# Kernel tuning notes

Hardware: AMD Instinct MI355X
Metric: run time of the kernel (lower is better)

## Reference

```python
import jax, jax.numpy as jnp
import numpy as np

ALPHA = 0.25
GAMMA = 2.0
IMG = 512.0


def _focal(t, logits):
    # faithful to get_focal_loss: sigmoid -> alpha/focal weighting -> BCE -> mean
    c = jax.nn.sigmoid(logits)
    alpha_factor = jnp.where(t == 1.0, ALPHA, 1.0 - ALPHA)
    focal_weight = alpha_factor * jnp.where(t == 1.0, 1.0 - c, c) ** GAMMA
    bce = -(t * jnp.log(c) + (1.0 - t) * jnp.log(1.0 - c))
    return (focal_weight * bce).mean()


def setup_inputs() -> dict:
    key = jax.random.key(0)
    kc, kr, kd, ka1, ka2, kb1, kb2, kl = jax.random.split(key, 8)
    B, A, C = 32, 200000, 10000
    classifications = jax.random.normal(kc, (B, C), dtype=jnp.float32)
    regressions = 0.1 * jax.random.normal(kr, (B, A, 4), dtype=jnp.float32)
    box_dist = jax.random.normal(kd, (B, A), dtype=jnp.float32)
    # anchors: random boxes inside a 512x512 image
    ctr = jax.random.uniform(ka1, (A, 2), minval=0.0, maxval=IMG)
    wh = jax.random.uniform(ka2, (A, 2), minval=16.0, maxval=256.0)
    anchor = jnp.concatenate([ctr - 0.5 * wh, ctr + 0.5 * wh], axis=1)
    anchors = anchor[None].astype(jnp.float32)  # [1, A, 4]
    # annotations: [B, 1, 7] = one gt box + 3 noun class indices (stored as float)
    gctr = jax.random.uniform(kb1, (B, 1, 2), minval=128.0, maxval=384.0)
    gwh = jax.random.uniform(kb2, (B, 1, 2), minval=64.0, maxval=256.0)
    gbox = jnp.concatenate([gctr - 0.5 * gwh, gctr + 0.5 * gwh], axis=2)
    nouns = jax.random.randint(kl, (B, 1, 3), 0, C).astype(jnp.float32)
    annotations = jnp.concatenate([gbox, nouns], axis=2).astype(jnp.float32)
    return {
        "classifications": classifications,
        "regressions": regressions,
        "box_dist": box_dist,
        "anchors": anchors,
        "annotations": annotations,
    }


def reference(classifications, regressions, box_dist, anchors, annotations):
    anchor = anchors[0]                              # [A, 4]
    aw = anchor[:, 2] - anchor[:, 0]
    ah = anchor[:, 3] - anchor[:, 1]
    ax = anchor[:, 0] + 0.5 * aw
    ay = anchor[:, 1] + 0.5 * ah
    area_a = aw * ah
    scale = jnp.array([0.1, 0.1, 0.2, 0.2], dtype=jnp.float32)

    def per_image(cls_j, reg_j, bd_j, ann_j):
        ann = ann_j[0]                               # [7] single annotation
        nouns = ann[4:7].astype(jnp.int32)
        target_nouns = jnp.zeros_like(cls_j).at[nouns].set(1.0)
        cls_loss = _focal(target_nouns, cls_j)
        # IoU of all anchors vs the single gt box; argmax over 1 box == box 0
        b = ann[:4]
        iw = jnp.clip(jnp.minimum(anchor[:, 2], b[2]) - jnp.maximum(anchor[:, 0], b[0]), 0.0)
        ih = jnp.clip(jnp.minimum(anchor[:, 3], b[3]) - jnp.maximum(anchor[:, 1], b[1]), 0.0)
        inter = iw * ih
        ua = jnp.clip(area_a + (b[2] - b[0]) * (b[3] - b[1]) - inter, 1e-8)
        iou_max = inter / ua                          # [A]
        pos = (iou_max >= 0.5).astype(cls_j.dtype)    # [A] float 0/1
        bbox_loss = _focal(pos, bd_j)
        # Faithful to the torch code: positive_indices.long() used as GATHER indices
        pidx = pos.astype(jnp.int32)                  # values in {0,1}
        aw_pi = aw[pidx]; ah_pi = ah[pidx]
        ax_pi = ax[pidx]; ay_pi = ay[pidx]
        # assigned_annotations rows are all identical (single gt, argmax==0),
        # so the 0/1 gather is an identity on the gt box
        gw_raw = b[2] - b[0]
        gh_raw = b[3] - b[1]
        gx = b[0] + 0.5 * gw_raw
        gy = b[1] + 0.5 * gh_raw
        gw = jnp.clip(gw_raw, 1.0)
        gh = jnp.clip(gh_raw, 1.0)
        targets = jnp.stack(
            [(gx - ax_pi) / aw_pi,
             (gy - ay_pi) / ah_pi,
             jnp.log(gw / aw_pi),
             jnp.log(gh / ah_pi)], axis=1) / scale    # [A, 4]
        diff = jnp.abs(targets - reg_j[pidx])
        rl = jnp.where(diff <= 1.0 / 9.0, 0.5 * 9.0 * diff ** 2, diff - 0.5 / 9.0).mean()
        reg_loss = jnp.where(pidx.sum() > 0, rl, jnp.zeros((), rl.dtype))
        return cls_loss, bbox_loss, reg_loss

    cl, bl, rl = jax.vmap(per_image)(classifications, regressions, box_dist, annotations)
    return (cl.mean(keepdims=True), bl.mean(keepdims=True), rl.mean(keepdims=True))
```

## Files before the change

kernel.cpp:

```cpp
#include <hip/hip_runtime.h>

#define B_IMG 32
#define N_A   200000
#define N_C   10000

#define NCH    60
#define BCH    3328
#define NCC    4
#define CCH    2560
#define SLOTS  64
#define GRID   (B_IMG * SLOTS)

#define WS_FOCAL 0
#define WS_CNT   (B_IMG * NCH)
#define WS_CLS   (2 * B_IMG * NCH)

typedef float f4 __attribute__((ext_vector_type(4)));

__device__ __forceinline__ float focal_elem(float x, bool t) {
    float e = __expf(-x);
    float r = __builtin_amdgcn_rcpf(1.0f + e);
    float L = __logf(1.0f + e);
    if (t) { float om = e * r; return 0.25f * om * om * L; }
    else   { return 0.75f * r * r * (x + L); }
}

__device__ __forceinline__ double wave_red(double v) {
#pragma unroll
    for (int o = 32; o; o >>= 1) v += __shfl_down(v, o, 64);
    return v;
}

__global__ __launch_bounds__(256) void main_kernel(
    const float* __restrict__ cls, const float* __restrict__ bd,
    const float* __restrict__ anc, const float* __restrict__ ann,
    double* __restrict__ ws)
{
    const int tid = threadIdx.x;
    const int lane = tid & 63, wv = tid >> 6;
    const int j  = blockIdx.x >> 6;
    const int ch = blockIdx.x & 63;
    __shared__ double sred[2][4];
    const f4* __restrict__ anc4 = (const f4*)anc;

    if (ch < NCH) {
        const int a0 = ch * BCH;
        const int a1 = (ch == NCH - 1) ? N_A : (a0 + BCH);
        const int nfull = (a1 - a0) >> 8;
        const float b0 = ann[j*7+0], b1 = ann[j*7+1], b2 = ann[j*7+2], b3 = ann[j*7+3];
        const float barea = (b2 - b0) * (b3 - b1);
        const float* __restrict__ bdr = bd + (size_t)j * N_A;

        float fsum = 0.0f, cnt = 0.0f;
        const int base = a0 + tid;
#pragma unroll 4
        for (int u = 0; u < nfull; ++u) {
            const int i = base + (u << 8);
            const f4 av = anc4[i];
            float iw = fmaxf(fminf(av.z, b2) - fmaxf(av.x, b0), 0.0f);
            float ih = fmaxf(fminf(av.w, b3) - fmaxf(av.y, b1), 0.0f);
            float inter = iw * ih;
            float ua = fmaxf((av.z - av.x) * (av.w - av.y) + barea - inter, 1e-8f);
            bool pos = (2.0f * inter >= ua);
            fsum += focal_elem(bdr[i], pos);
            cnt  += pos ? 1.0f : 0.0f;
        }
        {
            const int i = base + (nfull << 8);
            if (i < a1) {
                const f4 av = anc4[i];
                float iw = fmaxf(fminf(av.z, b2) - fmaxf(av.x, b0), 0.0f);
                float ih = fmaxf(fminf(av.w, b3) - fmaxf(av.y, b1), 0.0f);
                float inter = iw * ih;
                float ua = fmaxf((av.z - av.x) * (av.w - av.y) + barea - inter, 1e-8f);
                bool pos = (2.0f * inter >= ua);
                fsum += focal_elem(bdr[i], pos);
                cnt  += pos ? 1.0f : 0.0f;
            }
        }
        double fv = wave_red((double)fsum);
        double cv = wave_red((double)cnt);
        if (lane == 0) { sred[0][wv] = fv; sred[1][wv] = cv; }
        __syncthreads();
        if (tid == 0) {
            ws[WS_FOCAL + j * NCH + ch] = sred[0][0] + sred[0][1] + sred[0][2] + sred[0][3];
            ws[WS_CNT   + j * NCH + ch] = sred[1][0] + sred[1][1] + sred[1][2] + sred[1][3];
        }
    } else {
        const int cc = ch - NCH;
        const int c0 = cc * CCH;
        const int c1 = (cc == NCC - 1) ? N_C : (c0 + CCH);
        const int nfull = (c1 - c0) >> 8;
        const int n0 = (int)ann[j*7+4], n1 = (int)ann[j*7+5], n2 = (int)ann[j*7+6];
        const float* __restrict__ cj = cls + (size_t)j * N_C;
        float fsum = 0.0f;
        const int base = c0 + tid;
#pragma unroll 4
        for (int u = 0; u < nfull; ++u) {
            const int i = base + (u << 8);
            bool t = (i == n0) || (i == n1) || (i == n2);
            fsum += focal_elem(cj[i], t);
        }
        {
            const int i = base + (nfull << 8);
            if (i < c1) {
                bool t = (i == n0) || (i == n1) || (i == n2);
                fsum += focal_elem(cj[i], t);
            }
        }
        double v = wave_red((double)fsum);
        if (lane == 0) sred[0][wv] = v;
        __syncthreads();
        if (tid == 0)
            ws[WS_CLS + j * NCC + cc] = sred[0][0] + sred[0][1] + sred[0][2] + sred[0][3];
    }
}

__global__ void final_kernel(
    const float* __restrict__ anc, const float* __restrict__ ann,
    const float* __restrict__ reg, const double* __restrict__ ws,
    float* __restrict__ out)
{
    int t = threadIdx.x;
    double cl = 0.0, bl = 0.0, rl = 0.0;
    if (t < B_IMG) {
        int j = t;
        double fsum = 0.0, npos = 0.0, csum = 0.0;
#pragma unroll 10
        for (int c = 0; c < NCH; ++c) {
            fsum += ws[WS_FOCAL + j * NCH + c];
            npos += ws[WS_CNT   + j * NCH + c];
        }
#pragma unroll
        for (int c = 0; c < NCC; ++c) csum += ws[WS_CLS + j * NCC + c];
        cl = csum / (double)N_C;
        bl = fsum / (double)N_A;

        float b0 = ann[j*7+0], b1 = ann[j*7+1], b2 = ann[j*7+2], b3 = ann[j*7+3];
        float gw_raw = b2 - b0, gh_raw = b3 - b1;
        float gx = b0 + 0.5f * gw_raw, gy = b1 + 0.5f * gh_raw;
        float gw = fmaxf(gw_raw, 1.0f), gh = fmaxf(gh_raw, 1.0f);
        double s[2];
#pragma unroll
        for (int p = 0; p < 2; ++p) {
            float x0 = anc[p*4+0], y0 = anc[p*4+1], x1 = anc[p*4+2], y1 = anc[p*4+3];
            float aw = x1 - x0, ah = y1 - y0;
            float ax = x0 + 0.5f * aw, ay = y0 + 0.5f * ah;
            float tg[4];
            tg[0] = ((gx - ax) / aw) / 0.1f;
            tg[1] = ((gy - ay) / ah) / 0.1f;
            tg[2] = logf(gw / aw) / 0.2f;
            tg[3] = logf(gh / ah) / 0.2f;
            const float* rj = reg + (size_t)j * N_A * 4 + p * 4;
            double ssum = 0.0;
#pragma unroll
            for (int k = 0; k < 4; ++k) {
                float d = fabsf(tg[k] - rj[k]);
                float v = (d <= (1.0f / 9.0f)) ? (0.5f * 9.0f * d * d) : (d - 0.5f / 9.0f);
                ssum += (double)v;
            }
            s[p] = ssum;
        }
        double rlv = (((double)N_A - npos) * s[0] + npos * s[1]) / (4.0 * (double)N_A);
        rl = (npos > 0.0) ? rlv : 0.0;
    }
    cl = wave_red(cl);
    bl = wave_red(bl);
    rl = wave_red(rl);
    if (t == 0) {
        out[0] = (float)(cl / B_IMG);
        out[1] = (float)(bl / B_IMG);
        out[2] = (float)(rl / B_IMG);
    }
}

extern "C" void kernel_launch(void* const* d_in, const int* in_sizes, int n_in,
                              void* d_out, int out_size, void* d_ws, size_t ws_size,
                              hipStream_t stream) {
    const float* cls = (const float*)d_in[0];
    const float* reg = (const float*)d_in[1];
    const float* bd  = (const float*)d_in[2];
    const float* anc = (const float*)d_in[3];
    const float* ann = (const float*)d_in[4];
    float* out = (float*)d_out;
    double* ws = (double*)d_ws;

    hipLaunchKernelGGL(main_kernel, dim3(GRID), dim3(256), 0, stream,
                       cls, bd, anc, ann, ws);
    hipLaunchKernelGGL(final_kernel, dim3(1), dim3(64), 0, stream, anc, ann, reg, ws, out);
}
```

Measured before the change: 22.17 us.

## Fuse final reduction into main kernel via atomic last-block pattern

Replaces the separate final reduction kernel with a last-block-done pattern: each block atomically adds its partial sums into per-image double accumulators and bumps a counter, and the last block computes the final losses. The aim is to remove the second kernel launch and its serial tail. It adds a hipMemsetAsync to zero the workspace each call, contended double atomics, and relies on s_waitcnt ordering without an explicit fence. A memset node may cost as much as the launch it replaces.

```diff
diff --git a/kernel.cpp b/kernel.cpp
--- a/kernel.cpp
+++ b/kernel.cpp
@@ -11,9 +11,8 @@
 #define SLOTS  64
 #define GRID   (B_IMG * SLOTS)
 
-#define WS_FOCAL 0
-#define WS_CNT   (B_IMG * NCH)
-#define WS_CLS   (2 * B_IMG * NCH)
+#define WS_CTR_BYTES 1024
+#define WS_ZERO_BYTES 1028
 
 typedef float f4 __attribute__((ext_vector_type(4)));
 
@@ -31,16 +30,18 @@
     return v;
 }
 
-__global__ __launch_bounds__(256) void main_kernel(
+__global__ __launch_bounds__(256) void fused_kernel(
     const float* __restrict__ cls, const float* __restrict__ bd,
     const float* __restrict__ anc, const float* __restrict__ ann,
-    double* __restrict__ ws)
+    const float* __restrict__ reg, double* __restrict__ ws,
+    unsigned int* __restrict__ ctr, float* __restrict__ out)
 {
     const int tid = threadIdx.x;
     const int lane = tid & 63, wv = tid >> 6;
     const int j  = blockIdx.x >> 6;
     const int ch = blockIdx.x & 63;
     __shared__ double sred[2][4];
+    __shared__ int s_last;
     const f4* __restrict__ anc4 = (const f4*)anc;
 
     if (ch < NCH) {
@@ -83,8 +84,8 @@
         if (lane == 0) { sred[0][wv] = fv; sred[1][wv] = cv; }
         __syncthreads();
         if (tid == 0) {
-            ws[WS_FOCAL + j * NCH + ch] = sred[0][0] + sred[0][1] + sred[0][2] + sred[0][3];
-            ws[WS_CNT   + j * NCH + ch] = sred[1][0] + sred[1][1] + sred[1][2] + sred[1][3];
+            atomicAdd(&ws[j * 4 + 0], sred[0][0] + sred[0][1] + sred[0][2] + sred[0][3]);
+            atomicAdd(&ws[j * 4 + 1], sred[1][0] + sred[1][1] + sred[1][2] + sred[1][3]);
         }
     } else {
         const int cc = ch - NCH;
@@ -112,31 +113,27 @@
         if (lane == 0) sred[0][wv] = v;
         __syncthreads();
         if (tid == 0)
-            ws[WS_CLS + j * NCC + cc] = sred[0][0] + sred[0][1] + sred[0][2] + sred[0][3];
+            atomicAdd(&ws[j * 4 + 2], sred[0][0] + sred[0][1] + sred[0][2] + sred[0][3]);
     }
-}
 
-__global__ void final_kernel(
-    const float* __restrict__ anc, const float* __restrict__ ann,
-    const float* __restrict__ reg, const double* __restrict__ ws,
-    float* __restrict__ out)
-{
-    int t = threadIdx.x;
+    if (tid == 0) {
+        asm volatile("s_waitcnt vmcnt(0)" ::: "memory");
+        unsigned int old = atomicAdd(ctr, 1u);
+        s_last = (old == GRID - 1) ? 1 : 0;
+    }
+    __syncthreads();
+    if (!s_last) return;
+
     double cl = 0.0, bl = 0.0, rl = 0.0;
-    if (t < B_IMG) {
-        int j = t;
-        double fsum = 0.0, npos = 0.0, csum = 0.0;
-#pragma unroll 10
-        for (int c = 0; c < NCH; ++c) {
-            fsum += ws[WS_FOCAL + j * NCH + c];
-            npos += ws[WS_CNT   + j * NCH + c];
-        }
-#pragma unroll
-        for (int c = 0; c < NCC; ++c) csum += ws[WS_CLS + j * NCC + c];
+    if (tid < B_IMG) {
+        const int jj = tid;
+        double fsum = atomicAdd(&ws[jj * 4 + 0], 0.0);
+        double npos = atomicAdd(&ws[jj * 4 + 1], 0.0);
+        double csum = atomicAdd(&ws[jj * 4 + 2], 0.0);
         cl = csum / (double)N_C;
         bl = fsum / (double)N_A;
 
-        float b0 = ann[j*7+0], b1 = ann[j*7+1], b2 = ann[j*7+2], b3 = ann[j*7+3];
+        float b0 = ann[jj*7+0], b1 = ann[jj*7+1], b2 = ann[jj*7+2], b3 = ann[jj*7+3];
         float gw_raw = b2 - b0, gh_raw = b3 - b1;
         float gx = b0 + 0.5f * gw_raw, gy = b1 + 0.5f * gh_raw;
         float gw = fmaxf(gw_raw, 1.0f), gh = fmaxf(gh_raw, 1.0f);
@@ -151,7 +148,7 @@
             tg[1] = ((gy - ay) / ah) / 0.1f;
             tg[2] = logf(gw / aw) / 0.2f;
             tg[3] = logf(gh / ah) / 0.2f;
-            const float* rj = reg + (size_t)j * N_A * 4 + p * 4;
+            const float* rj = reg + (size_t)jj * N_A * 4 + p * 4;
             double ssum = 0.0;
 #pragma unroll
             for (int k = 0; k < 4; ++k) {
@@ -164,13 +161,15 @@
         double rlv = (((double)N_A - npos) * s[0] + npos * s[1]) / (4.0 * (double)N_A);
         rl = (npos > 0.0) ? rlv : 0.0;
     }
-    cl = wave_red(cl);
-    bl = wave_red(bl);
-    rl = wave_red(rl);
-    if (t == 0) {
-        out[0] = (float)(cl / B_IMG);
-        out[1] = (float)(bl / B_IMG);
-        out[2] = (float)(rl / B_IMG);
+    if (tid < 64) {
+        cl = wave_red(cl);
+        bl = wave_red(bl);
+        rl = wave_red(rl);
+        if (tid == 0) {
+            out[0] = (float)(cl / B_IMG);
+            out[1] = (float)(bl / B_IMG);
+            out[2] = (float)(rl / B_IMG);
+        }
     }
 }
 
@@ -184,8 +183,9 @@
     const float* ann = (const float*)d_in[4];
     float* out = (float*)d_out;
     double* ws = (double*)d_ws;
+    unsigned int* ctr = (unsigned int*)((char*)d_ws + WS_CTR_BYTES);
 
-    hipLaunchKernelGGL(main_kernel, dim3(GRID), dim3(256), 0, stream,
-                       cls, bd, anc, ann, ws);
-    hipLaunchKernelGGL(final_kernel, dim3(1), dim3(64), 0, stream, anc, ann, reg, ws, out);
+    hipMemsetAsync(d_ws, 0, WS_ZERO_BYTES, stream);
+    hipLaunchKernelGGL(fused_kernel, dim3(GRID), dim3(256), 0, stream,
+                       cls, bd, anc, ann, reg, ws, ctr, out);
 }
```

Result: slower. 42.48 us (+91.6%).
